# Kernel tuning notes

Measured on AMD Instinct MI355X. Metric: run time of the kernel, lower is better.

The kernel has to match this reference:

```python
import jax, jax.numpy as jnp
from jax import lax
import numpy as np

B, S, D, P = 32, 1024, 512, 20  # batch, seq_len, feature_dim, positioning_embedding


def setup_inputs() -> dict:
    key = jax.random.key(0)
    ks = jax.random.split(key, 10)
    s = 0.1  # param scale
    return {
        "x": jax.random.normal(ks[0], (B, S, D), jnp.float32),
        "pad_lengths": jnp.full((B,), S, dtype=jnp.int32),
        # LSTM params (torch gate order i,f,g,o)
        "W_ih": jax.random.normal(ks[1], (4 * P, D), jnp.float32) * s,
        "W_hh": jax.random.normal(ks[2], (4 * P, P), jnp.float32) * s,
        "b_ih": jax.random.normal(ks[3], (4 * P,), jnp.float32) * s,
        "b_hh": jax.random.normal(ks[4], (4 * P,), jnp.float32) * s,
        # mu_generator: Linear(P, 3); sigma_generator: Linear(P, 1)
        "W_mu": jax.random.normal(ks[5], (3, P), jnp.float32) * s,
        "b_mu": jax.random.normal(ks[6], (3,), jnp.float32) * s,
        "W_sigma": jax.random.normal(ks[7], (1, P), jnp.float32) * s,
        "b_sigma": jax.random.normal(ks[8], (1,), jnp.float32) * s,
    }


def _lstm(x, W_ih, W_hh, b_ih, b_hh):
    # x: [B, S, D] -> hidden states [B, S, P] (torch nn.LSTM, batch_first)
    b, _, _ = x.shape
    h0 = jnp.zeros((b, P), x.dtype)
    c0 = jnp.zeros((b, P), x.dtype)

    def step(carry, xt):
        h, c = carry
        gates = xt @ W_ih.T + h @ W_hh.T + b_ih + b_hh  # [B, 4P]
        i, f, g, o = jnp.split(gates, 4, axis=-1)
        i = jax.nn.sigmoid(i)
        f = jax.nn.sigmoid(f)
        g = jnp.tanh(g)
        o = jax.nn.sigmoid(o)
        c = f * c + i * g
        h = o * jnp.tanh(c)
        return (h, c), h

    _, hs = lax.scan(step, (h0, c0), jnp.swapaxes(x, 0, 1))  # hs: [S, B, P]
    return jnp.swapaxes(hs, 0, 1)


def reference(x, pad_lengths, W_ih, W_hh, b_ih, b_hh, W_mu, b_mu, W_sigma, b_sigma):
    b, s, _ = x.shape
    invL = 1.0 / pad_lengths.astype(jnp.float32)  # [B]

    pw = _lstm(x, W_ih, W_hh, b_ih, b_hh)                    # [B, S, P]
    mu_w = jax.nn.relu(pw @ W_mu.T + b_mu)                    # [B, S, 3]
    sigma = jax.nn.sigmoid(pw @ W_sigma.T + b_sigma)[..., 0]  # [B, S]

    # Sequential mu recurrence: mu_j = max(mw0*prev_mu + mw1/L + mw2*(j+1)/L, j/L)
    js = jnp.arange(s, dtype=jnp.float32)

    def mu_step(prev_mu, inp):
        mw, j = inp  # mw: [B, 3]
        mu = mw[:, 0] * prev_mu + mw[:, 1] * invL + mw[:, 2] * (j + 1.0) * invL
        mu = jnp.maximum(mu, j * invL)
        return mu, mu

    _, mus = lax.scan(mu_step, jnp.zeros((b,), jnp.float32),
                      (jnp.swapaxes(mu_w, 0, 1), js))  # mus: [S, B]
    mus = mus.T  # [B, S]

    # Gaussian attention over positions k/L, causal mask k <= j, L1 normalize
    pos = js[None, :] * invL[:, None]                         # [B, S] = k/L
    d2 = (pos[:, None, :] - mus[:, :, None]) ** 2             # [B, S(j), S(k)]
    w = jnp.exp(-d2 / (2.0 * sigma[:, :, None] ** 2 + 0.001))
    causal = jnp.tril(jnp.ones((s, s), jnp.float32))          # k <= j
    w = w * causal[None]
    w = w / jnp.maximum(jnp.sum(jnp.abs(w), axis=-1, keepdims=True), 1e-12)
    context = jnp.einsum('bjk,bkd->bjd', w, x)                # [B, S, D]
    return context
```

## Files before the change

### kernel.cpp

```cpp
#include <hip/hip_runtime.h>
#include <hip/hip_bf16.h>

#define B_ 32
#define S_ 1024
#define D_ 512
#define P_ 20
#define G_ 80

typedef __attribute__((ext_vector_type(8))) short short8v;
typedef __attribute__((ext_vector_type(4))) float f32x4;

__device__ __forceinline__ float sigm_f(float x) { return 1.f / (1.f + __expf(-x)); }
__device__ __forceinline__ float tanh_f(float x) { return 1.f - 2.f / (__expf(2.f * x) + 1.f); }
__device__ __forceinline__ unsigned short f2bf(float f) {
    unsigned int u = __float_as_uint(f);
    u += 0x7FFF + ((u >> 16) & 1);
    return (unsigned short)(u >> 16);
}
__device__ __forceinline__ float bcast(float v, int lane) {
    return __uint_as_float(__builtin_amdgcn_readlane(__float_as_uint(v), lane));
}
__device__ __forceinline__ short8v cvt8(float4 p, float4 q) {
    union { __hip_bfloat162 h2[4]; short8v s; } u;
    u.h2[0] = __float22bfloat162_rn(float2{p.x, p.y});
    u.h2[1] = __float22bfloat162_rn(float2{p.z, p.w});
    u.h2[2] = __float22bfloat162_rn(float2{q.x, q.y});
    u.h2[3] = __float22bfloat162_rn(float2{q.z, q.w});
    return u.s;
}

__global__ __launch_bounds__(256) void xw_kernel(const float* __restrict__ x,
                                                 const float* __restrict__ W_ih,
                                                 const float* __restrict__ b_ih,
                                                 const float* __restrict__ b_hh,
                                                 float* __restrict__ xw) {
    const int tid = threadIdx.x;
    const int w = tid >> 6, l = tid & 63;
    const int lo = l & 15, hi = l >> 4;
    const int m0 = blockIdx.x * 64 + w * 16;

    f32x4 acc[5];
#pragma unroll
    for (int n = 0; n < 5; ++n) acc[n] = (f32x4){0.f, 0.f, 0.f, 0.f};

    const float* xrow = x + (size_t)(m0 + lo) * D_ + hi * 8;
#pragma unroll 4
    for (int k0 = 0; k0 < D_; k0 += 32) {
        const float4 a0 = *(const float4*)(xrow + k0);
        const float4 a1 = *(const float4*)(xrow + k0 + 4);
        const short8v a = cvt8(a0, a1);
#pragma unroll
        for (int n = 0; n < 5; ++n) {
            const float* wr = W_ih + (size_t)(n * 16 + lo) * D_ + k0 + hi * 8;
            const float4 b0 = *(const float4*)(wr);
            const float4 b1 = *(const float4*)(wr + 4);
            const short8v bf = cvt8(b0, b1);
            acc[n] = __builtin_amdgcn_mfma_f32_16x16x32_bf16(a, bf, acc[n], 0, 0, 0);
        }
    }
#pragma unroll
    for (int n = 0; n < 5; ++n) {
        const int g = n * 16 + lo;
        const float bias = b_ih[g] + b_hh[g];
#pragma unroll
        for (int r = 0; r < 4; ++r) {
            const int m = m0 + hi * 4 + r;
            xw[(size_t)m * G_ + g] = acc[n][r] + bias;
        }
    }
}

__global__ __launch_bounds__(256) void conv_kernel(const float* __restrict__ x,
                                                   unsigned short* __restrict__ xT) {
    __shared__ unsigned short tile[64][80];
    const int b = blockIdx.z;
    const int s0 = blockIdx.x * 64;
    const int d0 = blockIdx.y * 64;
    const int t = threadIdx.x;
    const int r = t >> 2;
    const int c0 = (t & 3) * 16;

    const float4* src = (const float4*)(x + ((size_t)(b * S_ + s0 + r)) * D_ + d0 + c0);
    float4 v0 = src[0], v1 = src[1], v2 = src[2], v3 = src[3];
    float vv[16] = {v0.x, v0.y, v0.z, v0.w, v1.x, v1.y, v1.z, v1.w,
                    v2.x, v2.y, v2.z, v2.w, v3.x, v3.y, v3.z, v3.w};
#pragma unroll
    for (int e = 0; e < 16; ++e) tile[c0 + e][r] = f2bf(vv[e]);
    __syncthreads();

    const int dr = t >> 2;
    const int sc = (t & 3) * 16;
    const unsigned short* tr = &tile[dr][sc];
    uint4 w0 = *(const uint4*)(tr);
    uint4 w1 = *(const uint4*)(tr + 8);
    uint4* dst = (uint4*)(xT + ((size_t)(b * D_ + d0 + dr)) * S_ + s0 + sc);
    dst[0] = w0;
    dst[1] = w1;
}

__global__ __launch_bounds__(64) void lstm_kernel(const float* __restrict__ xw,
                                                  const float* __restrict__ W_hh,
                                                  const float* __restrict__ W_mu,
                                                  const float* __restrict__ b_mu,
                                                  const float* __restrict__ W_sig,
                                                  const float* __restrict__ b_sig,
                                                  const int* __restrict__ pad,
                                                  float* __restrict__ mus,
                                                  float* __restrict__ sigma) {
    const int b = blockIdx.x;
    const int l = threadIdx.x;
    __shared__ float mbuf[S_];
    __shared__ float sbuf[S_];

    float E[P_], F[P_];
#pragma unroll
    for (int q = 0; q < P_; ++q) { E[q] = 0.f; F[q] = 0.f; }
    if (l < P_) {
#pragma unroll
        for (int q = 0; q < P_; ++q) {
            E[q] = W_hh[(0 * P_ + l) * P_ + q];
            F[q] = W_hh[(1 * P_ + l) * P_ + q];
        }
    } else if (l < 23) {
#pragma unroll
        for (int q = 0; q < P_; ++q) E[q] = W_mu[(l - 20) * P_ + q];
    } else if (l == 23) {
#pragma unroll
        for (int q = 0; q < P_; ++q) E[q] = W_sig[q];
    } else if (l >= 32 && l < 32 + P_) {
        const int p = l - 32;
#pragma unroll
        for (int q = 0; q < P_; ++q) {
            E[q] = W_hh[(2 * P_ + p) * P_ + q];
            F[q] = W_hh[(3 * P_ + p) * P_ + q];
        }
    }

    const float invL = 1.f / (float)pad[b];
    const float hb = (l >= 20 && l < 23) ? b_mu[l - 20] : (l == 23 ? b_sig[0] : 0.f);
    const float ka = (l >= 32) ? 2.f : 1.f;
    const float Ka = (l >= 32) ? 2.f : 1.f;
    const float Kb = (l >= 32) ? -1.f : 0.f;
    const bool ld = (l < P_) || (l >= 32 && l < 32 + P_);
    const int o1 = (l < 32) ? l : (2 * P_ + (l - 32));
    const int o2 = (l < 32) ? (P_ + l) : (3 * P_ + (l - 32));

    float h = 0.f, c = 0.f, mu_prev = 0.f;
    const float* xwb = xw + (size_t)b * S_ * G_;

    float ri[8], rf[8];
#pragma unroll
    for (int u = 0; u < 8; ++u) {
        ri[u] = 0.f; rf[u] = 0.f;
        if (ld) {
            const float* r = xwb + (size_t)u * G_;
            ri[u] = r[o1]; rf[u] = r[o2];
        }
    }

    for (int T = 0; T < S_; T += 8) {
#pragma unroll
        for (int u = 0; u < 8; ++u) {
            const int t = T + u;
            float hq[P_];
#pragma unroll
            for (int q = 0; q < P_; ++q) hq[q] = bcast(h, q);

            float pa = 0.f, pb = 0.f, qa = 0.f, qb = 0.f;
#pragma unroll
            for (int q = 0; q < P_ / 2; ++q) {
                pa += E[q] * hq[q];            qa += F[q] * hq[q];
                pb += E[q + 10] * hq[q + 10];  qb += F[q + 10] * hq[q + 10];
            }
            const float d1 = pa + pb, d2 = qa + qb;
            const float arg1 = d1 + ri[u] + hb;
            const float arg2 = d2 + rf[u];

            const float s1 = sigm_f(ka * arg1);
            const float a1 = Ka * s1 + Kb;
            const float a2 = sigm_f(arg2);
            const float rv = fmaxf(arg1, 0.f);

            const float gx = __shfl_xor(a1, 32);
            const float ox = __shfl_xor(a2, 32);

            c = a2 * c + a1 * gx;
            h = ox * tanh_f(c);

            if (ld && t + 8 < S_) {
                const float* r = xwb + (size_t)(t + 8) * G_;
                ri[u] = r[o1]; rf[u] = r[o2];
            }
            if (t > 0) {
                if (l == 23) sbuf[t - 1] = s1;
                const float s0v = bcast(rv, 20);
                const float s1v = bcast(rv, 21);
                const float s2v = bcast(rv, 22);
                if (l == 0) {
                    const float j = (float)(t - 1);
                    float m = s0v * mu_prev + (s1v + s2v * (j + 1.f)) * invL;
                    m = fmaxf(m, j * invL);
                    mu_prev = m;
                    mbuf[t - 1] = m;
                }
            }
        }
    }
    {
        float hq[P_];
#pragma unroll
        for (int q = 0; q < P_; ++q) hq[q] = bcast(h, q);
        float pa = 0.f, pb = 0.f;
#pragma unroll
        for (int q = 0; q < P_ / 2; ++q) {
            pa += E[q] * hq[q];
            pb += E[q + 10] * hq[q + 10];
        }
        const float arg1 = pa + pb + hb;
        if (l == 23) sbuf[S_ - 1] = sigm_f(arg1);
        const float rv = fmaxf(arg1, 0.f);
        const float s0v = bcast(rv, 20);
        const float s1v = bcast(rv, 21);
        const float s2v = bcast(rv, 22);
        if (l == 0) {
            const float j = (float)(S_ - 1);
            float m = s0v * mu_prev + (s1v + s2v * (j + 1.f)) * invL;
            m = fmaxf(m, j * invL);
            mbuf[S_ - 1] = m;
        }
    }
    __builtin_amdgcn_s_waitcnt(0);
#pragma unroll
    for (int i = 0; i < S_ / (64 * 4); ++i) {
        const int idx = (i * 64 + l) * 4;
        *(float4*)&mus[(size_t)b * S_ + idx] = *(const float4*)&mbuf[idx];
        *(float4*)&sigma[(size_t)b * S_ + idx] = *(const float4*)&sbuf[idx];
    }
}

__global__ __launch_bounds__(256, 2) void attn_kernel(const unsigned short* __restrict__ xT,
                                                      const float* __restrict__ mus,
                                                      const float* __restrict__ sigma,
                                                      const int* __restrict__ pad,
                                                      float* __restrict__ out) {
    __shared__ unsigned short xt[D_][40];
    __shared__ float rsm[4][16];

    const int jt = (gridDim.x - 1) - blockIdx.x;
    const int b = blockIdx.y;
    const int tid = threadIdx.x;
    const int w = tid >> 6;
    const int l = tid & 63;
    const int lo = l & 15, hi = l >> 4;
    const int jw0 = jt * 64 + w * 16;
    const float invL = 1.f / (float)pad[b];

    const int jA = jw0 + lo;
    const float mu = mus[(size_t)b * S_ + jA];
    const float sg = sigma[(size_t)b * S_ + jA];
    const float nis = -1.f / (2.f * sg * sg + 0.001f);

    f32x4 acc[32];
#pragma unroll
    for (int dt = 0; dt < 32; ++dt) acc[dt] = (f32x4){0.f, 0.f, 0.f, 0.f};

    const unsigned short* xTb = xT + (size_t)b * D_ * S_;
    float rs = 0.f;
    const int kend = (jt + 1) * 64;

    for (int k0 = 0; k0 < kend; k0 += 32) {
        uint4 v[2][4];
#pragma unroll
        for (int rr = 0; rr < 2; ++rr) {
            const int d = tid + rr * 256;
            const uint4* src = (const uint4*)(xTb + (size_t)d * S_ + k0);
#pragma unroll
            for (int i = 0; i < 4; ++i) v[rr][i] = src[i];
        }
        __syncthreads();
#pragma unroll
        for (int rr = 0; rr < 2; ++rr) {
            const int d = tid + rr * 256;
#pragma unroll
            for (int i = 0; i < 4; ++i) *(uint4*)&xt[d][i * 8] = v[rr][i];
        }
        __syncthreads();

        short8v a;
#pragma unroll
        for (int e = 0; e < 8; ++e) {
            const int k = k0 + hi * 8 + e;
            const float dd = (float)k * invL - mu;
            const float wv = (k <= jA) ? __expf(dd * dd * nis) : 0.f;
            rs += wv;
            a[e] = (short)f2bf(wv);
        }
#pragma unroll
        for (int dt = 0; dt < 32; ++dt) {
            const short8v bf = *(const short8v*)&xt[dt * 16 + lo][hi * 8];
            acc[dt] = __builtin_amdgcn_mfma_f32_16x16x32_bf16(a, bf, acc[dt], 0, 0, 0);
        }
    }

    rs += __shfl_xor(rs, 16);
    rs += __shfl_xor(rs, 32);
    if (l < 16) rsm[w][l] = rs;
    __syncthreads();

#pragma unroll
    for (int r = 0; r < 4; ++r) {
        const int j = jw0 + hi * 4 + r;
        const float rcp = 1.f / fmaxf(rsm[w][hi * 4 + r], 1e-12f);
        float* ob = out + ((size_t)b * S_ + j) * D_ + lo;
#pragma unroll
        for (int dt = 0; dt < 32; ++dt) {
            ob[dt * 16] = acc[dt][r] * rcp;
        }
    }
}

extern "C" void kernel_launch(void* const* d_in, const int* in_sizes, int n_in,
                              void* d_out, int out_size, void* d_ws, size_t ws_size,
                              hipStream_t stream) {
    const float* x     = (const float*)d_in[0];
    const int*   pad   = (const int*)d_in[1];
    const float* W_ih  = (const float*)d_in[2];
    const float* W_hh  = (const float*)d_in[3];
    const float* b_ih  = (const float*)d_in[4];
    const float* b_hh  = (const float*)d_in[5];
    const float* W_mu  = (const float*)d_in[6];
    const float* b_mu  = (const float*)d_in[7];
    const float* W_sig = (const float*)d_in[8];
    const float* b_sig = (const float*)d_in[9];
    float* out = (float*)d_out;

    float* xw    = (float*)d_ws;
    float* mus   = xw + (size_t)B_ * S_ * G_;
    float* sigma = mus + (size_t)B_ * S_;
    unsigned short* xT = (unsigned short*)(sigma + (size_t)B_ * S_);

    xw_kernel<<<(B_ * S_) / 64, 256, 0, stream>>>(x, W_ih, b_ih, b_hh, xw);
    conv_kernel<<<dim3(S_ / 64, D_ / 64, B_), 256, 0, stream>>>(x, xT);
    lstm_kernel<<<B_, 64, 0, stream>>>(xw, W_hh, W_mu, b_mu, W_sig, b_sig, pad, mus, sigma);
    attn_kernel<<<dim3(S_ / 64, B_), 256, 0, stream>>>(xT, mus, sigma, pad, out);
}
```

Measured before the change: 753.4 us.

## Interleave four batch recurrences per wavefront in LSTM kernel

Each LSTM block now advances four independent batch sequences in one wavefront, interleaving their per-timestep work inside the unrolled loop. Previously each of the 32 single-wave blocks ran one latency-bound serial chain of readlanes, FMAs, exps and shuffles. Interleaving four chains gives the scheduler independent instructions to fill those stalls. In exchange, fewer blocks run (8 instead of 32), each wave does four times the instruction work per step, and register and shared memory use go up.

After: 1.714 ms. +127.4%, slower.

```diff
diff --git a/kernel.cpp b/kernel.cpp
--- a/kernel.cpp
+++ b/kernel.cpp
@@ -6,6 +6,7 @@
 #define D_ 512
 #define P_ 20
 #define G_ 80
+#define NC 4
 
 typedef __attribute__((ext_vector_type(8))) short short8v;
 typedef __attribute__((ext_vector_type(4))) float f32x4;
@@ -107,10 +108,10 @@
                                                   const int* __restrict__ pad,
                                                   float* __restrict__ mus,
                                                   float* __restrict__ sigma) {
-    const int b = blockIdx.x;
+    const int b0 = blockIdx.x * NC;
     const int l = threadIdx.x;
-    __shared__ float mbuf[S_];
-    __shared__ float sbuf[S_];
+    __shared__ float mbuf[NC][S_];
+    __shared__ float sbuf[NC][S_];
 
     float E[P_], F[P_];
 #pragma unroll
@@ -136,7 +137,6 @@
         }
     }
 
-    const float invL = 1.f / (float)pad[b];
     const float hb = (l >= 20 && l < 23) ? b_mu[l - 20] : (l == 23 ? b_sig[0] : 0.f);
     const float ka = (l >= 32) ? 2.f : 1.f;
     const float Ka = (l >= 32) ? 2.f : 1.f;
@@ -145,71 +145,82 @@
     const int o1 = (l < 32) ? l : (2 * P_ + (l - 32));
     const int o2 = (l < 32) ? (P_ + l) : (3 * P_ + (l - 32));
 
-    float h = 0.f, c = 0.f, mu_prev = 0.f;
-    const float* xwb = xw + (size_t)b * S_ * G_;
-
-    float ri[8], rf[8];
-#pragma unroll
-    for (int u = 0; u < 8; ++u) {
-        ri[u] = 0.f; rf[u] = 0.f;
-        if (ld) {
-            const float* r = xwb + (size_t)u * G_;
-            ri[u] = r[o1]; rf[u] = r[o2];
-        }
-    }
+    float invL[NC], h[NC], c[NC], mup[NC];
+    const float* xwb[NC];
+#pragma unroll
+    for (int j = 0; j < NC; ++j) {
+        invL[j] = 1.f / (float)pad[b0 + j];
+        h[j] = 0.f; c[j] = 0.f; mup[j] = 0.f;
+        xwb[j] = xw + (size_t)(b0 + j) * S_ * G_;
+    }
+
+    float ri[NC][8], rf[NC][8];
+#pragma unroll
+    for (int j = 0; j < NC; ++j)
+#pragma unroll
+        for (int u = 0; u < 8; ++u) {
+            ri[j][u] = 0.f; rf[j][u] = 0.f;
+            if (ld) {
+                const float* r = xwb[j] + (size_t)u * G_;
+                ri[j][u] = r[o1]; rf[j][u] = r[o2];
+            }
+        }
 
     for (int T = 0; T < S_; T += 8) {
 #pragma unroll
         for (int u = 0; u < 8; ++u) {
             const int t = T + u;
-            float hq[P_];
-#pragma unroll
-            for (int q = 0; q < P_; ++q) hq[q] = bcast(h, q);
-
-            float pa = 0.f, pb = 0.f, qa = 0.f, qb = 0.f;
-#pragma unroll
-            for (int q = 0; q < P_ / 2; ++q) {
-                pa += E[q] * hq[q];            qa += F[q] * hq[q];
-                pb += E[q + 10] * hq[q + 10];  qb += F[q + 10] * hq[q + 10];
-            }
-            const float d1 = pa + pb, d2 = qa + qb;
-            const float arg1 = d1 + ri[u] + hb;
-            const float arg2 = d2 + rf[u];
-
-            const float s1 = sigm_f(ka * arg1);
-            const float a1 = Ka * s1 + Kb;
-            const float a2 = sigm_f(arg2);
-            const float rv = fmaxf(arg1, 0.f);
-
-            const float gx = __shfl_xor(a1, 32);
-            const float ox = __shfl_xor(a2, 32);
-
-            c = a2 * c + a1 * gx;
-            h = ox * tanh_f(c);
-
-            if (ld && t + 8 < S_) {
-                const float* r = xwb + (size_t)(t + 8) * G_;
-                ri[u] = r[o1]; rf[u] = r[o2];
-            }
-            if (t > 0) {
-                if (l == 23) sbuf[t - 1] = s1;
-                const float s0v = bcast(rv, 20);
-                const float s1v = bcast(rv, 21);
-                const float s2v = bcast(rv, 22);
-                if (l == 0) {
-                    const float j = (float)(t - 1);
-                    float m = s0v * mu_prev + (s1v + s2v * (j + 1.f)) * invL;
-                    m = fmaxf(m, j * invL);
-                    mu_prev = m;
-                    mbuf[t - 1] = m;
+#pragma unroll
+            for (int j = 0; j < NC; ++j) {
+                float hq[P_];
+#pragma unroll
+                for (int q = 0; q < P_; ++q) hq[q] = bcast(h[j], q);
+
+                float pa = 0.f, pb = 0.f, qa = 0.f, qb = 0.f;
+#pragma unroll
+                for (int q = 0; q < P_ / 2; ++q) {
+                    pa += E[q] * hq[q];            qa += F[q] * hq[q];
+                    pb += E[q + 10] * hq[q + 10];  qb += F[q + 10] * hq[q + 10];
+                }
+                const float arg1 = pa + pb + ri[j][u] + hb;
+                const float arg2 = qa + qb + rf[j][u];
+
+                const float s1 = sigm_f(ka * arg1);
+                const float a1 = Ka * s1 + Kb;
+                const float a2 = sigm_f(arg2);
+                const float rv = fmaxf(arg1, 0.f);
+
+                const float gx = __shfl_xor(a1, 32);
+                const float ox = __shfl_xor(a2, 32);
+
+                c[j] = a2 * c[j] + a1 * gx;
+                h[j] = ox * tanh_f(c[j]);
+
+                if (ld && t + 8 < S_) {
+                    const float* r = xwb[j] + (size_t)(t + 8) * G_;
+                    ri[j][u] = r[o1]; rf[j][u] = r[o2];
+                }
+                if (t > 0) {
+                    if (l == 23) sbuf[j][t - 1] = s1;
+                    const float s0v = bcast(rv, 20);
+                    const float s1v = bcast(rv, 21);
+                    const float s2v = bcast(rv, 22);
+                    if (l == 0) {
+                        const float jj = (float)(t - 1);
+                        float m = s0v * mup[j] + (s1v + s2v * (jj + 1.f)) * invL[j];
+                        m = fmaxf(m, jj * invL[j]);
+                        mup[j] = m;
+                        mbuf[j][t - 1] = m;
+                    }
                 }
             }
         }
     }
-    {
+#pragma unroll
+    for (int j = 0; j < NC; ++j) {
         float hq[P_];
 #pragma unroll
-        for (int q = 0; q < P_; ++q) hq[q] = bcast(h, q);
+        for (int q = 0; q < P_; ++q) hq[q] = bcast(h[j], q);
         float pa = 0.f, pb = 0.f;
 #pragma unroll
         for (int q = 0; q < P_ / 2; ++q) {
@@ -217,25 +228,27 @@
             pb += E[q + 10] * hq[q + 10];
         }
         const float arg1 = pa + pb + hb;
-        if (l == 23) sbuf[S_ - 1] = sigm_f(arg1);
+        if (l == 23) sbuf[j][S_ - 1] = sigm_f(arg1);
         const float rv = fmaxf(arg1, 0.f);
         const float s0v = bcast(rv, 20);
         const float s1v = bcast(rv, 21);
         const float s2v = bcast(rv, 22);
         if (l == 0) {
-            const float j = (float)(S_ - 1);
-            float m = s0v * mu_prev + (s1v + s2v * (j + 1.f)) * invL;
-            m = fmaxf(m, j * invL);
-            mbuf[S_ - 1] = m;
+            const float jj = (float)(S_ - 1);
+            float m = s0v * mup[j] + (s1v + s2v * (jj + 1.f)) * invL[j];
+            m = fmaxf(m, jj * invL[j]);
+            mbuf[j][S_ - 1] = m;
         }
     }
     __builtin_amdgcn_s_waitcnt(0);
 #pragma unroll
-    for (int i = 0; i < S_ / (64 * 4); ++i) {
-        const int idx = (i * 64 + l) * 4;
-        *(float4*)&mus[(size_t)b * S_ + idx] = *(const float4*)&mbuf[idx];
-        *(float4*)&sigma[(size_t)b * S_ + idx] = *(const float4*)&sbuf[idx];
-    }
+    for (int j = 0; j < NC; ++j)
+#pragma unroll
+        for (int i = 0; i < S_ / (64 * 4); ++i) {
+            const int idx = (i * 64 + l) * 4;
+            *(float4*)&mus[(size_t)(b0 + j) * S_ + idx] = *(const float4*)&mbuf[j][idx];
+            *(float4*)&sigma[(size_t)(b0 + j) * S_ + idx] = *(const float4*)&sbuf[j][idx];
+        }
 }
 
 __global__ __launch_bounds__(256, 2) void attn_kernel(const unsigned short* __restrict__ xT,
@@ -341,6 +354,6 @@
 
     xw_kernel<<<(B_ * S_) / 64, 256, 0, stream>>>(x, W_ih, b_ih, b_hh, xw);
     conv_kernel<<<dim3(S_ / 64, D_ / 64, B_), 256, 0, stream>>>(x, xT);
-    lstm_kernel<<<B_, 64, 0, stream>>>(xw, W_hh, W_mu, b_mu, W_sig, b_sig, pad, mus, sigma);
+    lstm_kernel<<<B_ / NC, 64, 0, stream>>>(xw, W_hh, W_mu, b_mu, W_sig, b_sig, pad, mus, sigma);
     attn_kernel<<<dim3(S_ / 64, B_), 256, 0, stream>>>(xT, mus, sigma, pad, out);
 }
```
